# Optimization experiments

Hardware: AMD Instinct MI355X
Metric: run time of the kernel (lower is better)

The kernel has to match this reference:

```python
import jax, jax.numpy as jnp
import numpy as np

FP8_MAX = 448.0  # float8_e4m3fn max representable magnitude
AMAX_EPS = 1e-12


def _quantize_fp8_block(x):
    """Float8BlockQuantizer: 1D blocks of 128 along last dim (dim==128 => one
    block per row), force_pow_2_scales=True. Returns dequantized fp32 data
    (fp8 round-trip) and the per-block scale (rowwise_scale_inv)."""
    amax = jnp.maximum(jnp.max(jnp.abs(x), axis=-1, keepdims=True), AMAX_EPS)
    scale = jnp.exp2(jnp.ceil(jnp.log2(amax / FP8_MAX)))  # pow-2, >= amax/448
    xq = (x / scale).astype(jnp.float8_e4m3fn).astype(jnp.float32)
    return xq, scale[..., 0]


def setup_inputs() -> dict:
    key = jax.random.key(0)
    kq, kk, kw = jax.random.split(key, 3)
    seq_q, seq_k, head, dim = 4096, 4096, 32, 128
    return {
        "index_q": jax.random.normal(kq, (seq_q, head, dim), dtype=jnp.float32),
        "index_k": jax.random.normal(kk, (seq_k, dim), dtype=jnp.float32),
        "weights": jax.random.uniform(kw, (seq_q, head), dtype=jnp.float32),
        "index_topk": 2048,
        "chunk_offset": 0,
    }


def reference(index_q, index_k, weights, index_topk, chunk_offset):
    seq_q, head, dim = index_q.shape
    seq_k = index_k.shape[0]
    softmax_scale = dim ** (-0.5)

    qf, q_scale = _quantize_fp8_block(index_q)  # qf [sq,h,d], q_scale [sq,h]
    kf, k_scale = _quantize_fp8_block(index_k)  # kf [sk,d],   k_scale [sk]

    # fp8_mqa_logits: logits[i,j] = sum_h w_scaled[i,h] * (qf[i,h] . kf[j]) * k_scale[j]
    w_scaled = weights * q_scale * softmax_scale  # [sq,h]
    q_eff = jnp.einsum('qh,qhd->qd', w_scaled, qf)  # fold head-weighted sum
    logits = (q_eff @ kf.T) * k_scale[None, :]      # [sq, sk]

    # causal mask: valid keys are [k_start=0, k_end=i+chunk_offset+1)
    k_end = jnp.arange(seq_q, dtype=jnp.int32) + chunk_offset + 1
    mask = jnp.arange(seq_k, dtype=jnp.int32)[None, :] < k_end[:, None]
    logits = jnp.where(mask, logits, -jnp.inf)

    # index_topk <= seq_k here, so no padding branch needed
    vals, idx = jax.lax.top_k(logits, index_topk)  # sorted descending
    return vals, idx
```

## Files before the change

kernel.cpp:

```cpp
#include <hip/hip_runtime.h>
#include <stdint.h>

#define SQ 4096
#define SK 4096
#define NH 32
#define DIM 128
#define NBINS 16
#define HPAD 264


__device__ __forceinline__ float fp8_rt(float x) {
    int p = __builtin_amdgcn_cvt_pk_fp8_f32(x, x, 0, false);
    return __builtin_amdgcn_cvt_f32_fp8(p, 0);
}

__device__ __forceinline__ uint32_t map_f32(float v) {
    uint32_t b = __float_as_uint(v);
    return b ^ ((b & 0x80000000u) ? 0xFFFFFFFFu : 0x80000000u);
}

__device__ __forceinline__ void pow2_scale(float amax, float& scale, float& inv) {
    int e;
    float m = frexpf(amax, &e);
    int k = (m <= 0.875f) ? (e - 9) : (e - 8);
    scale = ldexpf(1.0f, k);
    inv = ldexpf(1.0f, -k);
}

__device__ __forceinline__ int vslot(int p) {
    return p ^ ((p >> 4) & 15) ^ ((p >> 8) & 15);
}

__global__ void prep_q(const float* __restrict__ q, const float* __restrict__ w,
                       float* __restrict__ q_eff) {
    int row = blockIdx.x;
    int t = threadIdx.x;
    const float softmax_scale = 0.08838834764831845f;
    float accx = 0.f, accy = 0.f;
    for (int h = 0; h < NH; ++h) {
        float2 v = *reinterpret_cast<const float2*>(q + ((size_t)row * NH + h) * DIM + 2 * t);
        float m = fmaxf(fabsf(v.x), fabsf(v.y));
#pragma unroll
        for (int off = 32; off > 0; off >>= 1) m = fmaxf(m, __shfl_xor(m, off));
        float amax = fmaxf(m, 1e-12f);
        float scale, inv;
        pow2_scale(amax, scale, inv);
        float ws = w[(size_t)row * NH + h] * scale * softmax_scale;
        accx += ws * fp8_rt(v.x * inv);
        accy += ws * fp8_rt(v.y * inv);
    }
    float2 o; o.x = accx; o.y = accy;
    *reinterpret_cast<float2*>(q_eff + (size_t)row * DIM + 2 * t) = o;
}

__global__ void prep_k(const float* __restrict__ kin, float* __restrict__ kfs) {
    int row = blockIdx.x;
    int t = threadIdx.x;
    float2 v = *reinterpret_cast<const float2*>(kin + (size_t)row * DIM + 2 * t);
    float m = fmaxf(fabsf(v.x), fabsf(v.y));
#pragma unroll
    for (int off = 32; off > 0; off >>= 1) m = fmaxf(m, __shfl_xor(m, off));
    float amax = fmaxf(m, 1e-12f);
    float scale, inv;
    pow2_scale(amax, scale, inv);
    float2 o; o.x = fp8_rt(v.x * inv) * scale; o.y = fp8_rt(v.y * inv) * scale;
    *reinterpret_cast<float2*>(kfs + (size_t)row * DIM + 2 * t) = o;
}

__global__ __launch_bounds__(256) void logits_radix_topk(
    const float* __restrict__ qe, const float* __restrict__ kfs,
    float* __restrict__ vals, int* __restrict__ idxs,
    const int* __restrict__ co_ptr, int topk) {
    __shared__ uint32_t sval[SK];
    __shared__ uint16_t sidx[SK];
    __shared__ uint16_t H[NBINS * HPAD];
    __shared__ uint32_t sbin[NBINS];
    __shared__ float qrow[DIM];

    int row = blockIdx.x;
    int t = threadIdx.x;
    int co = *co_ptr;
    int nv = row + co + 1;
    nv = nv < 0 ? 0 : (nv > SK ? SK : nv);
    int M = (nv + 15) & ~15;

    if (t < DIM / 4) {
        *reinterpret_cast<float4*>(qrow + t * 4) =
            *reinterpret_cast<const float4*>(qe + (size_t)row * DIM + t * 4);
    }
    __syncthreads();

    for (int i = 0; i < SK / 256; ++i) {
        int j = t + 256 * i;
        if (j < nv) {
            const float4* kp = reinterpret_cast<const float4*>(kfs + (size_t)j * DIM);
            float acc = 0.f;
#pragma unroll 8
            for (int d4 = 0; d4 < DIM / 4; ++d4) {
                float4 kv = kp[d4];
                float4 qv = *reinterpret_cast<const float4*>(qrow + d4 * 4);
                acc += qv.x * kv.x; acc += qv.y * kv.y;
                acc += qv.z * kv.z; acc += qv.w * kv.w;
            }
            sval[vslot(j)] = ~map_f32(acc);
        } else if (j < M) {
            sval[vslot(j)] = 0xFFFFFFFFu;
        }
    }
    __syncthreads();

    int base = t * 16;
    bool act = base < M;
    int wv = t >> 6, ln = t & 63;

    for (int pass = 0; pass < 8; ++pass) {
        int shift = pass * 4;
        uint32_t kb[16];
        uint32_t ib[16];
        uint32_t h0 = 0, h1 = 0, h2 = 0, h3 = 0;
        if (act) {
#pragma unroll
            for (int e = 0; e < 16; ++e) kb[e] = sval[vslot(base + e)];
            if (pass == 0) {
#pragma unroll
                for (int e = 0; e < 16; ++e) ib[e] = base + e;
            } else {
#pragma unroll
                for (int e = 0; e < 16; ++e) ib[e] = sidx[vslot(base + e)];
            }
#pragma unroll
            for (int e = 0; e < 16; ++e) {
                uint32_t d = (kb[e] >> shift) & 15u;
                uint32_t inc = 1u << ((d & 3u) << 3);
                uint32_t w = d >> 2;
                h0 += (w == 0) ? inc : 0u;
                h1 += (w == 1) ? inc : 0u;
                h2 += (w == 2) ? inc : 0u;
                h3 += (w == 3) ? inc : 0u;
            }
        }
#pragma unroll
        for (int b = 0; b < NBINS; ++b) {
            uint32_t hw = (b < 4) ? h0 : (b < 8) ? h1 : (b < 12) ? h2 : h3;
            H[b * HPAD + t] = (uint16_t)((hw >> ((b & 3) * 8)) & 0xFFu);
        }
        __syncthreads();

#pragma unroll
        for (int bb = 0; bb < 4; ++bb) {
            int b = wv * 4 + bb;
            uint32_t c0 = H[b * HPAD + 4 * ln + 0];
            uint32_t c1 = H[b * HPAD + 4 * ln + 1];
            uint32_t c2 = H[b * HPAD + 4 * ln + 2];
            uint32_t c3 = H[b * HPAD + 4 * ln + 3];
            uint32_t lsum = c0 + c1 + c2 + c3;
            uint32_t s = lsum;
#pragma unroll
            for (int off = 1; off < 64; off <<= 1) {
                uint32_t v = __shfl_up(s, off);
                if (ln >= off) s += v;
            }
            uint32_t excl = s - lsum;
            H[b * HPAD + 4 * ln + 0] = (uint16_t)excl;
            H[b * HPAD + 4 * ln + 1] = (uint16_t)(excl + c0);
            H[b * HPAD + 4 * ln + 2] = (uint16_t)(excl + c0 + c1);
            H[b * HPAD + 4 * ln + 3] = (uint16_t)(excl + c0 + c1 + c2);
            if (ln == 63) sbin[b] = s;
        }
        __syncthreads();

        if (t == 0) {
            uint32_t r = 0;
#pragma unroll
            for (int b = 0; b < NBINS; ++b) { uint32_t c = sbin[b]; sbin[b] = r; r += c; }
        }
        __syncthreads();

#pragma unroll
        for (int b = 0; b < NBINS; ++b)
            H[b * HPAD + t] = (uint16_t)(H[b * HPAD + t] + sbin[b]);

        if (act) {
            uint32_t c0 = 0, c1 = 0, c2 = 0, c3 = 0;
#pragma unroll
            for (int e = 0; e < 16; ++e) {
                uint32_t d = (kb[e] >> shift) & 15u;
                uint32_t w = d >> 2;
                uint32_t sh = (d & 3u) << 3;
                uint32_t colbase = H[d * HPAD + t];
                uint32_t cw = (w == 0) ? c0 : (w == 1) ? c1 : (w == 2) ? c2 : c3;
                uint32_t pos = colbase + ((cw >> sh) & 0xFFu);
                int sl = vslot((int)pos);
                sval[sl] = kb[e];
                sidx[sl] = (uint16_t)ib[e];
                uint32_t inc = 1u << sh;
                c0 += (w == 0) ? inc : 0u;
                c1 += (w == 1) ? inc : 0u;
                c2 += (w == 2) ? inc : 0u;
                c3 += (w == 3) ? inc : 0u;
            }
        }
        __syncthreads();
    }

    for (int n = t; n < topk; n += 256) {
        float v; int id;
        if (n < nv) {
            int sl = vslot(n);
            uint32_t m = ~sval[sl];
            uint32_t b = m ^ ((m & 0x80000000u) ? 0x80000000u : 0xFFFFFFFFu);
            v = __uint_as_float(b);
            id = (int)sidx[sl];
        } else {
            v = -1.0e30f;
            id = n;
        }
        if (!(fabsf(v) <= 1.0e38f)) v = -1.0e30f;
        vals[(size_t)row * topk + n] = v;
        idxs[(size_t)row * topk + n] = id;
    }
}

extern "C" void kernel_launch(void* const* d_in, const int* in_sizes, int n_in,
                              void* d_out, int out_size, void* d_ws, size_t ws_size,
                              hipStream_t stream) {
    (void)in_sizes; (void)n_in; (void)ws_size;
    const float* q = (const float*)d_in[0];
    const float* k = (const float*)d_in[1];
    const float* w = (const float*)d_in[2];
    const int* co_ptr = (const int*)d_in[4];
    int topk = out_size / (2 * SQ);

    char* ws = (char*)d_ws;
    float* q_eff = (float*)(ws);
    float* kfs   = (float*)(ws + (size_t)(2 << 20));

    hipLaunchKernelGGL(prep_q, dim3(SQ), dim3(64), 0, stream, q, w, q_eff);
    hipLaunchKernelGGL(prep_k, dim3(SK), dim3(64), 0, stream, k, kfs);
    hipLaunchKernelGGL(logits_radix_topk, dim3(SQ), dim3(256), 0, stream,
                       q_eff, kfs, (float*)d_out, (int*)d_out + (size_t)SQ * topk,
                       co_ptr, topk);
}
```

Baseline: 630.8 us.

## Pack key and index into 64-bit LDS entries and compute logits into registers

Sorting elements are now stored as packed 64-bit key|index words in one LDS array with a new swizzle, replacing separate 32-bit value and 16-bit index arrays. Each thread computes the dot products for its own 16 contiguous keys, four at a time, straight into registers, so the first radix pass skips the LDS round trip and one barrier. The serial bin-offset prefix by thread 0 and the per-column rewrite of H are replaced by a 16-lane shuffle scan whose result is added at scatter time. The cost is twice the LDS bytes per element, and each thread now reads four strided key rows at once, which may load global memory less efficiently than before.

```diff
diff --git a/kernel.cpp b/kernel.cpp
--- a/kernel.cpp
+++ b/kernel.cpp
@@ -7,6 +7,7 @@
 #define DIM 128
 #define NBINS 16
 #define HPAD 264
+#define CHUNK 16
 
 
 __device__ __forceinline__ float fp8_rt(float x) {
@@ -27,8 +28,10 @@
     inv = ldexpf(1.0f, -k);
 }
 
-__device__ __forceinline__ int vslot(int p) {
-    return p ^ ((p >> 4) & 15) ^ ((p >> 8) & 15);
+__device__ __forceinline__ int eslot(int p) {
+    int q = p >> 1;
+    q ^= (q >> 3) & 7;
+    return q * 2 + (p & 1);
 }
 
 __global__ void prep_q(const float* __restrict__ q, const float* __restrict__ w,
@@ -71,8 +74,7 @@
     const float* __restrict__ qe, const float* __restrict__ kfs,
     float* __restrict__ vals, int* __restrict__ idxs,
     const int* __restrict__ co_ptr, int topk) {
-    __shared__ uint32_t sval[SK];
-    __shared__ uint16_t sidx[SK];
+    __shared__ __align__(16) uint64_t ev[SK];
     __shared__ uint16_t H[NBINS * HPAD];
     __shared__ uint32_t sbin[NBINS];
     __shared__ float qrow[DIM];
@@ -82,7 +84,7 @@
     int co = *co_ptr;
     int nv = row + co + 1;
     nv = nv < 0 ? 0 : (nv > SK ? SK : nv);
-    int M = (nv + 15) & ~15;
+    int M = (nv + CHUNK - 1) & ~(CHUNK - 1);
 
     if (t < DIM / 4) {
         *reinterpret_cast<float4*>(qrow + t * 4) =
@@ -90,47 +92,63 @@
     }
     __syncthreads();
 
-    for (int i = 0; i < SK / 256; ++i) {
-        int j = t + 256 * i;
-        if (j < nv) {
-            const float4* kp = reinterpret_cast<const float4*>(kfs + (size_t)j * DIM);
-            float acc = 0.f;
+    int base = t * CHUNK;
+    bool act = base < M;
+    uint64_t kb[CHUNK];
+#pragma unroll
+    for (int e0 = 0; e0 < CHUNK; e0 += 4) {
+        int j0 = base + e0;
+        if (j0 < nv) {
+            int j1 = (j0 + 1 < nv) ? j0 + 1 : 0;
+            int j2 = (j0 + 2 < nv) ? j0 + 2 : 0;
+            int j3 = (j0 + 3 < nv) ? j0 + 3 : 0;
+            const float4* p0 = reinterpret_cast<const float4*>(kfs + (size_t)j0 * DIM);
+            const float4* p1 = reinterpret_cast<const float4*>(kfs + (size_t)j1 * DIM);
+            const float4* p2 = reinterpret_cast<const float4*>(kfs + (size_t)j2 * DIM);
+            const float4* p3 = reinterpret_cast<const float4*>(kfs + (size_t)j3 * DIM);
+            float a0 = 0.f, a1 = 0.f, a2 = 0.f, a3 = 0.f;
 #pragma unroll 8
             for (int d4 = 0; d4 < DIM / 4; ++d4) {
-                float4 kv = kp[d4];
                 float4 qv = *reinterpret_cast<const float4*>(qrow + d4 * 4);
-                acc += qv.x * kv.x; acc += qv.y * kv.y;
-                acc += qv.z * kv.z; acc += qv.w * kv.w;
-            }
-            sval[vslot(j)] = ~map_f32(acc);
-        } else if (j < M) {
-            sval[vslot(j)] = 0xFFFFFFFFu;
-        }
-    }
-    __syncthreads();
-
-    int base = t * 16;
-    bool act = base < M;
+                float4 k0 = p0[d4], k1 = p1[d4], k2 = p2[d4], k3 = p3[d4];
+                a0 += qv.x * k0.x; a0 += qv.y * k0.y; a0 += qv.z * k0.z; a0 += qv.w * k0.w;
+                a1 += qv.x * k1.x; a1 += qv.y * k1.y; a1 += qv.z * k1.z; a1 += qv.w * k1.w;
+                a2 += qv.x * k2.x; a2 += qv.y * k2.y; a2 += qv.z * k2.z; a2 += qv.w * k2.w;
+                a3 += qv.x * k3.x; a3 += qv.y * k3.y; a3 += qv.z * k3.z; a3 += qv.w * k3.w;
+            }
+            float ar[4] = {a0, a1, a2, a3};
+#pragma unroll
+            for (int r = 0; r < 4; ++r) {
+                int j = j0 + r;
+                kb[e0 + r] = (j < nv)
+                    ? (((uint64_t)(~map_f32(ar[r])) << 32) | (uint32_t)j)
+                    : ~0ULL;
+            }
+        } else {
+#pragma unroll
+            for (int r = 0; r < 4; ++r) kb[e0 + r] = ~0ULL;
+        }
+    }
+
     int wv = t >> 6, ln = t & 63;
 
     for (int pass = 0; pass < 8; ++pass) {
         int shift = pass * 4;
-        uint32_t kb[16];
-        uint32_t ib[16];
+        if (pass > 0 && act) {
+#pragma unroll
+            for (int f = 0; f < CHUNK / 2; ++f) {
+                int q = (base >> 1) + f;
+                int q2 = q ^ ((q >> 3) & 7);
+                ulonglong2 v = *reinterpret_cast<const ulonglong2*>(&ev[q2 * 2]);
+                kb[2 * f] = v.x;
+                kb[2 * f + 1] = v.y;
+            }
+        }
         uint32_t h0 = 0, h1 = 0, h2 = 0, h3 = 0;
         if (act) {
 #pragma unroll
-            for (int e = 0; e < 16; ++e) kb[e] = sval[vslot(base + e)];
-            if (pass == 0) {
-#pragma unroll
-                for (int e = 0; e < 16; ++e) ib[e] = base + e;
-            } else {
-#pragma unroll
-                for (int e = 0; e < 16; ++e) ib[e] = sidx[vslot(base + e)];
-            }
-#pragma unroll
-            for (int e = 0; e < 16; ++e) {
-                uint32_t d = (kb[e] >> shift) & 15u;
+            for (int e = 0; e < CHUNK; ++e) {
+                uint32_t d = ((uint32_t)(kb[e] >> 32) >> shift) & 15u;
                 uint32_t inc = 1u << ((d & 3u) << 3);
                 uint32_t w = d >> 2;
                 h0 += (w == 0) ? inc : 0u;
@@ -169,30 +187,28 @@
         }
         __syncthreads();
 
-        if (t == 0) {
-            uint32_t r = 0;
-#pragma unroll
-            for (int b = 0; b < NBINS; ++b) { uint32_t c = sbin[b]; sbin[b] = r; r += c; }
-        }
-        __syncthreads();
-
-#pragma unroll
-        for (int b = 0; b < NBINS; ++b)
-            H[b * HPAD + t] = (uint16_t)(H[b * HPAD + t] + sbin[b]);
+        if (wv == 0 && ln < NBINS) {
+            uint32_t s = sbin[ln];
+            uint32_t lsum = s;
+#pragma unroll
+            for (int off = 1; off < NBINS; off <<= 1) {
+                uint32_t v = __shfl_up(s, off);
+                if (ln >= off) s += v;
+            }
+            sbin[ln] = s - lsum;
+        }
+        __syncthreads();
 
         if (act) {
             uint32_t c0 = 0, c1 = 0, c2 = 0, c3 = 0;
 #pragma unroll
-            for (int e = 0; e < 16; ++e) {
-                uint32_t d = (kb[e] >> shift) & 15u;
+            for (int e = 0; e < CHUNK; ++e) {
+                uint32_t d = ((uint32_t)(kb[e] >> 32) >> shift) & 15u;
                 uint32_t w = d >> 2;
                 uint32_t sh = (d & 3u) << 3;
-                uint32_t colbase = H[d * HPAD + t];
                 uint32_t cw = (w == 0) ? c0 : (w == 1) ? c1 : (w == 2) ? c2 : c3;
-                uint32_t pos = colbase + ((cw >> sh) & 0xFFu);
-                int sl = vslot((int)pos);
-                sval[sl] = kb[e];
-                sidx[sl] = (uint16_t)ib[e];
+                uint32_t pos = sbin[d] + H[d * HPAD + t] + ((cw >> sh) & 0xFFu);
+                ev[eslot((int)pos)] = kb[e];
                 uint32_t inc = 1u << sh;
                 c0 += (w == 0) ? inc : 0u;
                 c1 += (w == 1) ? inc : 0u;
@@ -206,11 +222,11 @@
     for (int n = t; n < topk; n += 256) {
         float v; int id;
         if (n < nv) {
-            int sl = vslot(n);
-            uint32_t m = ~sval[sl];
+            uint64_t kk = ev[eslot(n)];
+            uint32_t m = ~(uint32_t)(kk >> 32);
             uint32_t b = m ^ ((m & 0x80000000u) ? 0x80000000u : 0xFFFFFFFFu);
             v = __uint_as_float(b);
-            id = (int)sidx[sl];
+            id = (int)(uint32_t)kk;
         } else {
             v = -1.0e30f;
             id = n;
```

After: 723.6 us. +14.7%, slower.
